# Optimization experiments

Measured on AMD Instinct MI355X. Metric: run time of the kernel, lower is better.

The kernel has to match this reference:

```python
import jax, jax.numpy as jnp
import numpy as np

DIM_IN = 1024
DIM_OUT = 1024
NUM_HEADS = 16
HEAD_DIM = DIM_OUT // NUM_HEADS


def setup_inputs() -> dict:
    key = jax.random.key(0)
    ks = jax.random.split(key, 7)
    s = 1.0 / np.sqrt(DIM_IN)
    x = jax.random.normal(ks[0], (4, 2048, DIM_IN), dtype=jnp.float32)
    Wq = jax.random.uniform(ks[1], (DIM_IN, DIM_OUT), jnp.float32, -s, s)
    bq = jax.random.uniform(ks[2], (DIM_OUT,), jnp.float32, -s, s)
    Wk = jax.random.uniform(ks[3], (DIM_IN, DIM_OUT), jnp.float32, -s, s)
    bk = jax.random.uniform(ks[4], (DIM_OUT,), jnp.float32, -s, s)
    Wv = jax.random.uniform(ks[5], (DIM_IN, DIM_OUT), jnp.float32, -s, s)
    bv = jax.random.uniform(ks[6], (DIM_OUT,), jnp.float32, -s, s)
    return {"x": x, "Wq": Wq, "bq": bq, "Wk": Wk, "bk": bk, "Wv": Wv, "bv": bv}


def reference(x, Wq, bq, Wk, bk, Wv, bv):
    B, S, _ = x.shape
    scale = HEAD_DIM ** 0.5
    # project and split heads: [B, H, S, Dh]
    def heads(W, b):
        return (x @ W + b).reshape(B, S, NUM_HEADS, HEAD_DIM).transpose(0, 2, 1, 3)
    q = heads(Wq, bq)
    k = heads(Wk, bk)
    v = heads(Wv, bv)
    scores = jnp.einsum("bhqd,bhkd->bhqk", q, k) / scale  # [B,H,S,S]
    attn = jax.nn.softmax(scores, axis=-1)
    out = jnp.einsum("bhqk,bhkd->bhqd", attn, v)
    return out.transpose(0, 2, 1, 3).reshape(B, S, DIM_OUT)
```

## Files before the change

### kernel.cpp

```cpp
#include <hip/hip_runtime.h>
#include <hip/hip_bf16.h>


#define DIM  1024
#define SEQ  2048
#define BATCH 4
#define NH   16
#define HD   64

typedef __bf16 bf16x8 __attribute__((ext_vector_type(8)));
typedef short  s16x4  __attribute__((ext_vector_type(4)));
typedef float  f32x4  __attribute__((ext_vector_type(4)));
typedef float  f32x16 __attribute__((ext_vector_type(16)));
typedef unsigned int uint4v __attribute__((ext_vector_type(4)));

static __device__ __forceinline__ f32x16 mfma32(bf16x8 a, bf16x8 b, f32x16 c) {
    return __builtin_amdgcn_mfma_f32_32x32x16_bf16(a, b, c, 0, 0, 0);
}

static __device__ __forceinline__ unsigned short f2b(float f) {
    __bf16 h = (__bf16)f;
    return __builtin_bit_cast(unsigned short, h);
}

static __device__ __forceinline__ void load_lds16(const unsigned short* g,
                                                  unsigned short* l) {
    __builtin_amdgcn_global_load_lds(
        (const __attribute__((address_space(1))) void*)g,
        (__attribute__((address_space(3))) void*)l, 16, 0, 0);
}

__global__ __launch_bounds__(256) void cvt_x_k(const float* __restrict__ x,
                                               unsigned short* __restrict__ xb) {
    size_t i = ((size_t)blockIdx.x * 256 + threadIdx.x) * 8;
    const f32x4* s = (const f32x4*)(x + i);
    f32x4 a0 = s[0], a1 = s[1];
    bf16x8 v;
    for (int j = 0; j < 4; j++) { v[j] = (__bf16)a0[j]; v[4 + j] = (__bf16)a1[j]; }
    *(bf16x8*)(xb + i) = v;
}

__global__ void transpose_w_k(const float* __restrict__ Wq,
                              const float* __restrict__ Wk,
                              const float* __restrict__ Wv,
                              unsigned short* __restrict__ Wt) {
    __shared__ unsigned short t[32][33];
    int z = blockIdx.z;
    const float* W = (z == 0) ? Wq : (z == 1) ? Wk : Wv;
    unsigned short* o = Wt + (size_t)z * DIM * DIM;
    int tx = threadIdx.x;
    int n0 = blockIdx.x * 32, k0 = blockIdx.y * 32;
    for (int j = threadIdx.y; j < 32; j += 8)
        t[j][tx] = f2b(W[(size_t)(k0 + j) * DIM + n0 + tx]);
    __syncthreads();
    for (int j = threadIdx.y; j < 32; j += 8)
        o[(size_t)(n0 + j) * DIM + k0 + tx] = t[tx][j];
}

__global__ __launch_bounds__(512) void qkv_gemm_k(
    const unsigned short* __restrict__ xb,
    const unsigned short* __restrict__ WtBase,
    const float* __restrict__ bq,
    const float* __restrict__ bk,
    const float* __restrict__ bv,
    unsigned short* __restrict__ Qo,
    unsigned short* __restrict__ Ko,
    unsigned short* __restrict__ Vto) {
    __shared__ __align__(16) unsigned short As[256 * 64];
    __shared__ __align__(16) unsigned short Bs[128 * 64];
    int tid = threadIdx.x, wave = tid >> 6, lane = tid & 63;
    int quad = lane >> 4, lc = lane & 15;
    int bid = blockIdx.x;
    int xcd = bid & 7, slot = bid >> 3;
    int pp = slot / 24, i = slot - pp * 24;
    int p = pp * 8 + xcd;
    int z = i >> 3, nx = i & 7;
    int m0 = p * 256, n0 = nx * 128;
    const unsigned short* Wt = WtBase + (size_t)z * DIM * DIM;
    int wm = (wave >> 1) * 64, wn = (wave & 1) * 64;
    int swzlo = lc & 7;

    f32x4 acc[4][4] = {};

    for (int k0 = 0; k0 < DIM; k0 += 64) {
        __syncthreads();
        #pragma unroll
        for (int pI = 0; pI < 4; pI++) {
            int c = tid + pI * 512, r = c >> 3, cc = (c & 7) ^ (r & 7);
            load_lds16(xb + (size_t)(m0 + r) * DIM + k0 + cc * 8, &As[c * 8]);
        }
        #pragma unroll
        for (int pI = 0; pI < 2; pI++) {
            int c = tid + pI * 512, r = c >> 3, cc = (c & 7) ^ (r & 7);
            load_lds16(Wt + (size_t)(n0 + r) * DIM + k0 + cc * 8, &Bs[c * 8]);
        }
        __syncthreads();
        #pragma unroll
        for (int kk = 0; kk < 2; kk++) {
            int off = ((kk * 4 + quad) ^ swzlo) * 8;
            bf16x8 af[4], bfr[4];
            for (int mt = 0; mt < 4; mt++)
                af[mt] = *(const bf16x8*)&As[(wm + mt * 16 + lc) * 64 + off];
            for (int nt = 0; nt < 4; nt++)
                bfr[nt] = *(const bf16x8*)&Bs[(wn + nt * 16 + lc) * 64 + off];
            for (int mt = 0; mt < 4; mt++)
                for (int nt = 0; nt < 4; nt++)
                    acc[mt][nt] = __builtin_amdgcn_mfma_f32_16x16x32_bf16(
                        af[mt], bfr[nt], acc[mt][nt], 0, 0, 0);
        }
    }

    const float* bias = (z == 0) ? bq : (z == 1) ? bk : bv;
    float scale = (z == 0) ? 0.18033688011112042f : 1.0f;

    if (z != 2) {
        for (int nt = 0; nt < 4; nt++) {
            int n = n0 + wn + nt * 16 + lc;
            float bvl = bias[n];
            int h = n >> 6, d = n & 63;
            for (int mt = 0; mt < 4; mt++) {
                for (int r = 0; r < 4; r++) {
                    int m = m0 + wm + mt * 16 + quad * 4 + r;
                    int b = m >> 11, s = m & 2047;
                    unsigned short ub = f2b((acc[mt][nt][r] + bvl) * scale);
                    if (z == 0)
                        Qo[((size_t)(b * NH + h) * SEQ + s) * HD + d] = ub;
                    else
                        Ko[((size_t)(b * NH + h) * SEQ + s) * HD + d] = ub;
                }
            }
        }
    } else {
        __syncthreads();
        unsigned short* T = As + wave * 1024;
        int h = (n0 + wn) >> 6;
        int d = lane;
        for (int mt = 0; mt < 4; mt++) {
            for (int nt = 0; nt < 4; nt++) {
                int n = n0 + wn + nt * 16 + lc;
                float bvl = bias[n];
                s16x4 v4;
                for (int r = 0; r < 4; r++)
                    v4[r] = (short)f2b(acc[mt][nt][r] + bvl);
                *(s16x4*)&T[(nt * 16 + lc) * 16 + quad * 4] = v4;
            }
            int s_base = m0 + wm + mt * 16;
            int b = s_base >> 11, sl = s_base & 2047;
            unsigned short* dst =
                Vto + ((size_t)(b * NH + h) * HD + d) * SEQ + sl;
            uint4v t0 = *(const uint4v*)&T[d * 16];
            uint4v t1 = *(const uint4v*)&T[d * 16 + 8];
            *(uint4v*)&dst[0] = t0;
            *(uint4v*)&dst[8] = t1;
        }
    }
}

__global__ __launch_bounds__(512) void attn_k(
    const unsigned short* __restrict__ Q,
    const unsigned short* __restrict__ K,
    const unsigned short* __restrict__ Vt,
    float* __restrict__ out) {
    __shared__ __align__(16) unsigned short KV[2 * 8192];

    int tid = threadIdx.x, wave = tid >> 6, lane = tid & 63;
    int l31 = lane & 31, hi = lane >> 5;
    int bid = blockIdx.x;
    int j = bid >> 3;
    int bh = (bid & 7) * 8 + (j >> 3);
    int qt = j & 7;
    int b = bh >> 4, h = bh & 15;
    const unsigned short* Qg = Q + ((size_t)bh * SEQ + qt * 256) * HD;
    const unsigned short* Kg = K + (size_t)bh * SEQ * HD;
    const unsigned short* Vg = Vt + (size_t)bh * HD * SEQ;

    int sr = tid >> 3, scc = tid & 7;
    int kcc = scc ^ ((sr ^ (sr >> 3)) & 7);

    bf16x8 qf[4];
    {
        const unsigned short* q0 = Qg + (size_t)(wave * 32 + l31) * HD + hi * 8;
        #pragma unroll
        for (int ds_ = 0; ds_ < 4; ds_++)
            qf[ds_] = *(const bf16x8*)(q0 + ds_ * 16);
    }

    f32x16 o[2] = {};
    f32x16 racc = {};
    bf16x8 ones8;
    #pragma unroll
    for (int t = 0; t < 8; t++) ones8[t] = (__bf16)1.0f;

    int swzK0 = ((l31 ^ (l31 >> 3)) & 7);
    int r32 = 32 + l31;
    int swzK1 = ((r32 ^ (r32 >> 3)) & 7);

    {
        unsigned short* Ks = KV;
        unsigned short* Vs = KV + 4096;
        load_lds16(Kg + (size_t)sr * HD + kcc * 8, &Ks[tid * 8]);
        load_lds16(Vg + (size_t)sr * SEQ + kcc * 8, &Vs[tid * 8]);
    }

    for (int t0 = 0; t0 < SEQ; t0 += 64) {
        int cur = (t0 >> 6) & 1;
        unsigned short* Ks = KV + cur * 8192;
        unsigned short* Vs = Ks + 4096;
        __syncthreads();

        if (t0 + 64 < SEQ) {
            unsigned short* Kn = KV + (cur ^ 1) * 8192;
            unsigned short* Vn = Kn + 4096;
            load_lds16(Kg + (size_t)(t0 + 64 + sr) * HD + kcc * 8, &Kn[tid * 8]);
            load_lds16(Vg + (size_t)sr * SEQ + (t0 + 64) + kcc * 8, &Vn[tid * 8]);
        }

        __builtin_amdgcn_s_setprio(1);
        #pragma unroll
        for (int kb = 0; kb < 2; kb++) {
            int krow = kb * 32 + l31;
            int ksw = (kb == 0) ? swzK0 : swzK1;
            f32x16 sc = {};
            #pragma unroll
            for (int ds_ = 0; ds_ < 4; ds_++) {
                bf16x8 kfrag = *(const bf16x8*)
                    &Ks[krow * 64 + ((ds_ * 2 + hi) ^ ksw) * 8];
                sc = mfma32(kfrag, qf[ds_], sc);
            }
            unsigned int W[8];
            #pragma unroll
            for (int rr = 0; rr < 8; rr++) {
                float p0 = __builtin_amdgcn_exp2f(sc[2 * rr]);
                float p1 = __builtin_amdgcn_exp2f(sc[2 * rr + 1]);
                W[rr] = ((unsigned)f2b(p1) << 16) | (unsigned)f2b(p0);
            }
            asm volatile("v_permlane32_swap_b32 %0, %1"
                         : "+v"(W[0]), "+v"(W[2]));
            asm volatile("v_permlane32_swap_b32 %0, %1"
                         : "+v"(W[1]), "+v"(W[3]));
            asm volatile("v_permlane32_swap_b32 %0, %1"
                         : "+v"(W[4]), "+v"(W[6]));
            asm volatile("v_permlane32_swap_b32 %0, %1"
                         : "+v"(W[5]), "+v"(W[7]));
            bf16x8 fA = __builtin_bit_cast(bf16x8,
                            (uint4v){W[0], W[1], W[2], W[3]});
            bf16x8 fB = __builtin_bit_cast(bf16x8,
                            (uint4v){W[4], W[5], W[6], W[7]});
            racc = mfma32(ones8, fA, racc);
            racc = mfma32(ones8, fB, racc);
            #pragma unroll
            for (int db = 0; db < 2; db++) {
                int vrow = db * 32 + l31;
                int vsw = (db == 0) ? swzK0 : swzK1;
                bf16x8 v0 = *(const bf16x8*)
                    &Vs[vrow * 64 + ((kb * 4 + hi) ^ vsw) * 8];
                bf16x8 v1 = *(const bf16x8*)
                    &Vs[vrow * 64 + ((kb * 4 + 2 + hi) ^ vsw) * 8];
                o[db] = mfma32(v0, fA, o[db]);
                o[db] = mfma32(v1, fB, o[db]);
            }
        }
        __builtin_amdgcn_s_setprio(0);
    }

    float inv = 1.0f / racc[0];

    float* orow = out + ((size_t)b * SEQ + qt * 256 + wave * 32 + l31) * DIM
                  + h * HD + hi * 4;
    #pragma unroll
    for (int db = 0; db < 2; db++) {
        #pragma unroll
        for (int rr = 0; rr < 4; rr++) {
            f32x4 s = { o[db][4 * rr], o[db][4 * rr + 1],
                        o[db][4 * rr + 2], o[db][4 * rr + 3] };
            s *= inv;
            *(f32x4*)&orow[db * 32 + rr * 8] = s;
        }
    }
}

extern "C" void kernel_launch(void* const* d_in, const int* in_sizes, int n_in,
                              void* d_out, int out_size, void* d_ws, size_t ws_size,
                              hipStream_t stream) {
    (void)in_sizes; (void)n_in; (void)out_size; (void)ws_size;
    const float* x  = (const float*)d_in[0];
    const float* Wq = (const float*)d_in[1];
    const float* bq = (const float*)d_in[2];
    const float* Wk = (const float*)d_in[3];
    const float* bk = (const float*)d_in[4];
    const float* Wv = (const float*)d_in[5];
    const float* bv = (const float*)d_in[6];

    char* ws = (char*)d_ws;
    unsigned short* Wt = (unsigned short*)ws;
    unsigned short* Qb = (unsigned short*)(ws + (size_t)6 * 1024 * 1024);
    unsigned short* Kb = Qb + (size_t)BATCH * NH * SEQ * HD;
    unsigned short* Vb = Kb + (size_t)BATCH * NH * SEQ * HD;
    unsigned short* xb = (unsigned short*)d_out;

    cvt_x_k<<<dim3(4096), dim3(256), 0, stream>>>(x, xb);
    transpose_w_k<<<dim3(32, 32, 3), dim3(32, 8), 0, stream>>>(Wq, Wk, Wv, Wt);
    qkv_gemm_k<<<dim3(768), dim3(512), 0, stream>>>(xb, Wt, bq, bk, bv, Qb, Kb, Vb);
    attn_k<<<dim3(512), dim3(512), 0, stream>>>(Qb, Kb, Vb, (float*)d_out);
}
```

Baseline: 239.8 us.

## Double attention KV tile to 128 keys and merge prep kernels into one launch

The attention kernel now stages 128 keys per iteration instead of 64, with 64KB of LDS for the double buffer, a new V swizzle over 16 chunks per row, and half as many barriers per sequence. The x conversion and weight transpose kernels are fused into a single launch, removing one kernel-launch gap. The bf16 packing of P now uses a vector cast, which may let the compiler emit a packed convert. The larger LDS footprint may lower occupancy of the attention kernel.

After: 237.1 us. About the same (-1.1%).

```diff
diff --git a/kernel.cpp b/kernel.cpp
--- a/kernel.cpp
+++ b/kernel.cpp
@@ -9,6 +9,7 @@
 #define HD   64
 
 typedef __bf16 bf16x8 __attribute__((ext_vector_type(8)));
+typedef __bf16 bf16x2 __attribute__((ext_vector_type(2)));
 typedef short  s16x4  __attribute__((ext_vector_type(4)));
 typedef float  f32x4  __attribute__((ext_vector_type(4)));
 typedef float  f32x16 __attribute__((ext_vector_type(16)));
@@ -30,31 +31,33 @@
         (__attribute__((address_space(3))) void*)l, 16, 0, 0);
 }
 
-__global__ __launch_bounds__(256) void cvt_x_k(const float* __restrict__ x,
-                                               unsigned short* __restrict__ xb) {
-    size_t i = ((size_t)blockIdx.x * 256 + threadIdx.x) * 8;
-    const f32x4* s = (const f32x4*)(x + i);
-    f32x4 a0 = s[0], a1 = s[1];
-    bf16x8 v;
-    for (int j = 0; j < 4; j++) { v[j] = (__bf16)a0[j]; v[4 + j] = (__bf16)a1[j]; }
-    *(bf16x8*)(xb + i) = v;
-}
-
-__global__ void transpose_w_k(const float* __restrict__ Wq,
-                              const float* __restrict__ Wk,
-                              const float* __restrict__ Wv,
-                              unsigned short* __restrict__ Wt) {
+__global__ __launch_bounds__(256) void prep_k(
+    const float* __restrict__ x, unsigned short* __restrict__ xb,
+    const float* __restrict__ Wq, const float* __restrict__ Wk,
+    const float* __restrict__ Wv, unsigned short* __restrict__ Wt) {
     __shared__ unsigned short t[32][33];
-    int z = blockIdx.z;
-    const float* W = (z == 0) ? Wq : (z == 1) ? Wk : Wv;
-    unsigned short* o = Wt + (size_t)z * DIM * DIM;
-    int tx = threadIdx.x;
-    int n0 = blockIdx.x * 32, k0 = blockIdx.y * 32;
-    for (int j = threadIdx.y; j < 32; j += 8)
-        t[j][tx] = f2b(W[(size_t)(k0 + j) * DIM + n0 + tx]);
-    __syncthreads();
-    for (int j = threadIdx.y; j < 32; j += 8)
-        o[(size_t)(n0 + j) * DIM + k0 + tx] = t[tx][j];
+    int bid = blockIdx.x, tid = threadIdx.x;
+    if (bid < 4096) {
+        size_t i = ((size_t)bid * 256 + tid) * 8;
+        const f32x4* s = (const f32x4*)(x + i);
+        f32x4 a0 = s[0], a1 = s[1];
+        bf16x8 v;
+        for (int j = 0; j < 4; j++) { v[j] = (__bf16)a0[j]; v[4 + j] = (__bf16)a1[j]; }
+        *(bf16x8*)(xb + i) = v;
+    } else {
+        int r = bid - 4096;
+        int z = r >> 10;
+        int by = (r >> 5) & 31, bx = r & 31;
+        const float* W = (z == 0) ? Wq : (z == 1) ? Wk : Wv;
+        unsigned short* o = Wt + (size_t)z * DIM * DIM;
+        int tx = tid & 31, ty = tid >> 5;
+        int n0 = bx * 32, k0 = by * 32;
+        for (int j = ty; j < 32; j += 8)
+            t[j][tx] = f2b(W[(size_t)(k0 + j) * DIM + n0 + tx]);
+        __syncthreads();
+        for (int j = ty; j < 32; j += 8)
+            o[(size_t)(n0 + j) * DIM + k0 + tx] = t[tx][j];
+    }
 }
 
 __global__ __launch_bounds__(512) void qkv_gemm_k(
@@ -161,7 +164,7 @@
     const unsigned short* __restrict__ K,
     const unsigned short* __restrict__ Vt,
     float* __restrict__ out) {
-    __shared__ __align__(16) unsigned short KV[2 * 8192];
+    __shared__ __align__(16) unsigned short KV[2 * 16384];
 
     int tid = threadIdx.x, wave = tid >> 6, lane = tid & 63;
     int l31 = lane & 31, hi = lane >> 5;
@@ -174,8 +177,14 @@
     const unsigned short* Kg = K + (size_t)bh * SEQ * HD;
     const unsigned short* Vg = Vt + (size_t)bh * HD * SEQ;
 
-    int sr = tid >> 3, scc = tid & 7;
-    int kcc = scc ^ ((sr ^ (sr >> 3)) & 7);
+    int kr0 = tid >> 3, kc0 = tid & 7;
+    int ks0 = kc0 ^ ((kr0 ^ (kr0 >> 3)) & 7);
+    int kr1 = (tid + 512) >> 3, kc1 = tid & 7;
+    int ks1 = kc1 ^ ((kr1 ^ (kr1 >> 3)) & 7);
+    int vr0 = tid >> 4, vc0 = tid & 15;
+    int vs0 = (vc0 & 8) | ((vc0 & 7) ^ ((vr0 ^ (vr0 >> 3)) & 7));
+    int vr1 = (tid + 512) >> 4, vc1 = tid & 15;
+    int vs1 = (vc1 & 8) | ((vc1 & 7) ^ ((vr1 ^ (vr1 >> 3)) & 7));
 
     bf16x8 qf[4];
     {
@@ -197,29 +206,37 @@
 
     {
         unsigned short* Ks = KV;
-        unsigned short* Vs = KV + 4096;
-        load_lds16(Kg + (size_t)sr * HD + kcc * 8, &Ks[tid * 8]);
-        load_lds16(Vg + (size_t)sr * SEQ + kcc * 8, &Vs[tid * 8]);
-    }
-
-    for (int t0 = 0; t0 < SEQ; t0 += 64) {
-        int cur = (t0 >> 6) & 1;
-        unsigned short* Ks = KV + cur * 8192;
-        unsigned short* Vs = Ks + 4096;
-        __syncthreads();
-
-        if (t0 + 64 < SEQ) {
-            unsigned short* Kn = KV + (cur ^ 1) * 8192;
-            unsigned short* Vn = Kn + 4096;
-            load_lds16(Kg + (size_t)(t0 + 64 + sr) * HD + kcc * 8, &Kn[tid * 8]);
-            load_lds16(Vg + (size_t)sr * SEQ + (t0 + 64) + kcc * 8, &Vn[tid * 8]);
+        unsigned short* Vs = KV + 8192;
+        load_lds16(Kg + (size_t)kr0 * HD + ks0 * 8, &Ks[tid * 8]);
+        load_lds16(Kg + (size_t)kr1 * HD + ks1 * 8, &Ks[(tid + 512) * 8]);
+        load_lds16(Vg + (size_t)vr0 * SEQ + vs0 * 8, &Vs[tid * 8]);
+        load_lds16(Vg + (size_t)vr1 * SEQ + vs1 * 8, &Vs[(tid + 512) * 8]);
+    }
+
+    for (int t0 = 0; t0 < SEQ; t0 += 128) {
+        int cur = (t0 >> 7) & 1;
+        unsigned short* Ks = KV + cur * 16384;
+        unsigned short* Vs = Ks + 8192;
+        __syncthreads();
+
+        if (t0 + 128 < SEQ) {
+            unsigned short* Kn = KV + (cur ^ 1) * 16384;
+            unsigned short* Vn = Kn + 8192;
+            load_lds16(Kg + (size_t)(t0 + 128 + kr0) * HD + ks0 * 8,
+                       &Kn[tid * 8]);
+            load_lds16(Kg + (size_t)(t0 + 128 + kr1) * HD + ks1 * 8,
+                       &Kn[(tid + 512) * 8]);
+            load_lds16(Vg + (size_t)vr0 * SEQ + (t0 + 128) + vs0 * 8,
+                       &Vn[tid * 8]);
+            load_lds16(Vg + (size_t)vr1 * SEQ + (t0 + 128) + vs1 * 8,
+                       &Vn[(tid + 512) * 8]);
         }
 
         __builtin_amdgcn_s_setprio(1);
         #pragma unroll
-        for (int kb = 0; kb < 2; kb++) {
+        for (int kb = 0; kb < 4; kb++) {
             int krow = kb * 32 + l31;
-            int ksw = (kb == 0) ? swzK0 : swzK1;
+            int ksw = (kb & 1) ? swzK1 : swzK0;
             f32x16 sc = {};
             #pragma unroll
             for (int ds_ = 0; ds_ < 4; ds_++) {
@@ -232,7 +249,8 @@
             for (int rr = 0; rr < 8; rr++) {
                 float p0 = __builtin_amdgcn_exp2f(sc[2 * rr]);
                 float p1 = __builtin_amdgcn_exp2f(sc[2 * rr + 1]);
-                W[rr] = ((unsigned)f2b(p1) << 16) | (unsigned)f2b(p0);
+                bf16x2 pk; pk[0] = (__bf16)p0; pk[1] = (__bf16)p1;
+                W[rr] = __builtin_bit_cast(unsigned int, pk);
             }
             asm volatile("v_permlane32_swap_b32 %0, %1"
                          : "+v"(W[0]), "+v"(W[2]));
@@ -252,10 +270,11 @@
             for (int db = 0; db < 2; db++) {
                 int vrow = db * 32 + l31;
                 int vsw = (db == 0) ? swzK0 : swzK1;
-                bf16x8 v0 = *(const bf16x8*)
-                    &Vs[vrow * 64 + ((kb * 4 + hi) ^ vsw) * 8];
-                bf16x8 v1 = *(const bf16x8*)
-                    &Vs[vrow * 64 + ((kb * 4 + 2 + hi) ^ vsw) * 8];
+                int rawA = kb * 4 + hi, rawB = kb * 4 + 2 + hi;
+                int cA = (rawA & 8) | ((rawA & 7) ^ vsw);
+                int cB = (rawB & 8) | ((rawB & 7) ^ vsw);
+                bf16x8 v0 = *(const bf16x8*)&Vs[vrow * 128 + cA * 8];
+                bf16x8 v1 = *(const bf16x8*)&Vs[vrow * 128 + cB * 8];
                 o[db] = mfma32(v0, fA, o[db]);
                 o[db] = mfma32(v1, fB, o[db]);
             }
@@ -298,8 +317,7 @@
     unsigned short* Vb = Kb + (size_t)BATCH * NH * SEQ * HD;
     unsigned short* xb = (unsigned short*)d_out;
 
-    cvt_x_k<<<dim3(4096), dim3(256), 0, stream>>>(x, xb);
-    transpose_w_k<<<dim3(32, 32, 3), dim3(32, 8), 0, stream>>>(Wq, Wk, Wv, Wt);
+    prep_k<<<dim3(7168), dim3(256), 0, stream>>>(x, xb, Wq, Wk, Wv, Wt);
     qkv_gemm_k<<<dim3(768), dim3(512), 0, stream>>>(xb, Wt, bq, bk, bv, Qb, Kb, Vb);
     attn_k<<<dim3(512), dim3(512), 0, stream>>>(Qb, Kb, Vb, (float*)d_out);
 }
```

## Double-buffer QKV GEMM LDS with K-step 32, merge prep kernels, pack bf16

Applied to the files above, without the earlier changes.

The QKV projection GEMM now uses two LDS buffers with a K-step of 32 and a matching swizzle. The next tile is prefetched while MFMAs run on the current one, which drops one barrier per iteration. The x conversion and weight transpose kernels are merged into one launch to save launch overhead. The attention kernel now packs exp results with a native bf16x2 conversion. Risks: a smaller K-step doubles the loop iterations, and the single-barrier scheme depends on asynchronous LDS loads completing before the barrier.

New measurement: 239.3 us. Within noise of the previous version (-0.2%).

```diff
diff --git a/kernel.cpp b/kernel.cpp
--- a/kernel.cpp
+++ b/kernel.cpp
@@ -9,6 +9,7 @@
 #define HD   64
 
 typedef __bf16 bf16x8 __attribute__((ext_vector_type(8)));
+typedef __bf16 bf16x2 __attribute__((ext_vector_type(2)));
 typedef short  s16x4  __attribute__((ext_vector_type(4)));
 typedef float  f32x4  __attribute__((ext_vector_type(4)));
 typedef float  f32x16 __attribute__((ext_vector_type(16)));
@@ -30,31 +31,33 @@
         (__attribute__((address_space(3))) void*)l, 16, 0, 0);
 }
 
-__global__ __launch_bounds__(256) void cvt_x_k(const float* __restrict__ x,
-                                               unsigned short* __restrict__ xb) {
-    size_t i = ((size_t)blockIdx.x * 256 + threadIdx.x) * 8;
-    const f32x4* s = (const f32x4*)(x + i);
-    f32x4 a0 = s[0], a1 = s[1];
-    bf16x8 v;
-    for (int j = 0; j < 4; j++) { v[j] = (__bf16)a0[j]; v[4 + j] = (__bf16)a1[j]; }
-    *(bf16x8*)(xb + i) = v;
-}
-
-__global__ void transpose_w_k(const float* __restrict__ Wq,
-                              const float* __restrict__ Wk,
-                              const float* __restrict__ Wv,
-                              unsigned short* __restrict__ Wt) {
+__global__ __launch_bounds__(256) void prep_k(
+    const float* __restrict__ x, unsigned short* __restrict__ xb,
+    const float* __restrict__ Wq, const float* __restrict__ Wk,
+    const float* __restrict__ Wv, unsigned short* __restrict__ Wt) {
     __shared__ unsigned short t[32][33];
-    int z = blockIdx.z;
-    const float* W = (z == 0) ? Wq : (z == 1) ? Wk : Wv;
-    unsigned short* o = Wt + (size_t)z * DIM * DIM;
-    int tx = threadIdx.x;
-    int n0 = blockIdx.x * 32, k0 = blockIdx.y * 32;
-    for (int j = threadIdx.y; j < 32; j += 8)
-        t[j][tx] = f2b(W[(size_t)(k0 + j) * DIM + n0 + tx]);
-    __syncthreads();
-    for (int j = threadIdx.y; j < 32; j += 8)
-        o[(size_t)(n0 + j) * DIM + k0 + tx] = t[tx][j];
+    int bid = blockIdx.x, tid = threadIdx.x;
+    if (bid < 4096) {
+        size_t i = ((size_t)bid * 256 + tid) * 8;
+        const f32x4* s = (const f32x4*)(x + i);
+        f32x4 a0 = s[0], a1 = s[1];
+        bf16x8 v;
+        for (int j = 0; j < 4; j++) { v[j] = (__bf16)a0[j]; v[4 + j] = (__bf16)a1[j]; }
+        *(bf16x8*)(xb + i) = v;
+    } else {
+        int r = bid - 4096;
+        int z = r >> 10;
+        int by = (r >> 5) & 31, bx = r & 31;
+        const float* W = (z == 0) ? Wq : (z == 1) ? Wk : Wv;
+        unsigned short* o = Wt + (size_t)z * DIM * DIM;
+        int tx = tid & 31, ty = tid >> 5;
+        int n0 = bx * 32, k0 = by * 32;
+        for (int j = ty; j < 32; j += 8)
+            t[j][tx] = f2b(W[(size_t)(k0 + j) * DIM + n0 + tx]);
+        __syncthreads();
+        for (int j = ty; j < 32; j += 8)
+            o[(size_t)(n0 + j) * DIM + k0 + tx] = t[tx][j];
+    }
 }
 
 __global__ __launch_bounds__(512) void qkv_gemm_k(
@@ -66,8 +69,7 @@
     unsigned short* __restrict__ Qo,
     unsigned short* __restrict__ Ko,
     unsigned short* __restrict__ Vto) {
-    __shared__ __align__(16) unsigned short As[256 * 64];
-    __shared__ __align__(16) unsigned short Bs[128 * 64];
+    __shared__ __align__(16) unsigned short AB[2 * 12288];
     int tid = threadIdx.x, wave = tid >> 6, lane = tid & 63;
     int quad = lane >> 4, lc = lane & 15;
     int bid = blockIdx.x;
@@ -78,36 +80,52 @@
     int m0 = p * 256, n0 = nx * 128;
     const unsigned short* Wt = WtBase + (size_t)z * DIM * DIM;
     int wm = (wave >> 1) * 64, wn = (wave & 1) * 64;
-    int swzlo = lc & 7;
+    int off = ((quad ^ ((lc >> 1) & 3))) * 8;
+
+    int ar0 = tid >> 2, ac0 = (tid & 3) ^ ((ar0 >> 1) & 3);
+    int ar1 = (tid + 512) >> 2, ac1 = (tid & 3) ^ ((ar1 >> 1) & 3);
+    int br0 = tid >> 2, bc0 = (tid & 3) ^ ((br0 >> 1) & 3);
 
     f32x4 acc[4][4] = {};
 
-    for (int k0 = 0; k0 < DIM; k0 += 64) {
+    {
+        unsigned short* As = AB;
+        unsigned short* Bs = AB + 8192;
+        load_lds16(xb + (size_t)(m0 + ar0) * DIM + ac0 * 8, &As[tid * 8]);
+        load_lds16(xb + (size_t)(m0 + ar1) * DIM + ac1 * 8, &As[(tid + 512) * 8]);
+        load_lds16(Wt + (size_t)(n0 + br0) * DIM + bc0 * 8, &Bs[tid * 8]);
+    }
+
+    for (int k0 = 0; k0 < DIM; k0 += 32) {
+        int cur = (k0 >> 5) & 1;
+        unsigned short* As = AB + cur * 12288;
+        unsigned short* Bs = As + 8192;
         __syncthreads();
-        #pragma unroll
-        for (int pI = 0; pI < 4; pI++) {
-            int c = tid + pI * 512, r = c >> 3, cc = (c & 7) ^ (r & 7);
-            load_lds16(xb + (size_t)(m0 + r) * DIM + k0 + cc * 8, &As[c * 8]);
-        }
-        #pragma unroll
-        for (int pI = 0; pI < 2; pI++) {
-            int c = tid + pI * 512, r = c >> 3, cc = (c & 7) ^ (r & 7);
-            load_lds16(Wt + (size_t)(n0 + r) * DIM + k0 + cc * 8, &Bs[c * 8]);
-        }
-        __syncthreads();
-        #pragma unroll
-        for (int kk = 0; kk < 2; kk++) {
-            int off = ((kk * 4 + quad) ^ swzlo) * 8;
-            bf16x8 af[4], bfr[4];
-            for (int mt = 0; mt < 4; mt++)
-                af[mt] = *(const bf16x8*)&As[(wm + mt * 16 + lc) * 64 + off];
+
+        if (k0 + 32 < DIM) {
+            unsigned short* An = AB + (cur ^ 1) * 12288;
+            unsigned short* Bn = An + 8192;
+            load_lds16(xb + (size_t)(m0 + ar0) * DIM + k0 + 32 + ac0 * 8,
+                       &An[tid * 8]);
+            load_lds16(xb + (size_t)(m0 + ar1) * DIM + k0 + 32 + ac1 * 8,
+                       &An[(tid + 512) * 8]);
+            load_lds16(Wt + (size_t)(n0 + br0) * DIM + k0 + 32 + bc0 * 8,
+                       &Bn[tid * 8]);
+        }
+
+        bf16x8 af[4], bfr[4];
+        #pragma unroll
+        for (int mt = 0; mt < 4; mt++)
+            af[mt] = *(const bf16x8*)&As[(wm + mt * 16 + lc) * 32 + off];
+        #pragma unroll
+        for (int nt = 0; nt < 4; nt++)
+            bfr[nt] = *(const bf16x8*)&Bs[(wn + nt * 16 + lc) * 32 + off];
+        #pragma unroll
+        for (int mt = 0; mt < 4; mt++)
+            #pragma unroll
             for (int nt = 0; nt < 4; nt++)
-                bfr[nt] = *(const bf16x8*)&Bs[(wn + nt * 16 + lc) * 64 + off];
-            for (int mt = 0; mt < 4; mt++)
-                for (int nt = 0; nt < 4; nt++)
-                    acc[mt][nt] = __builtin_amdgcn_mfma_f32_16x16x32_bf16(
-                        af[mt], bfr[nt], acc[mt][nt], 0, 0, 0);
-        }
+                acc[mt][nt] = __builtin_amdgcn_mfma_f32_16x16x32_bf16(
+                    af[mt], bfr[nt], acc[mt][nt], 0, 0, 0);
     }
 
     const float* bias = (z == 0) ? bq : (z == 1) ? bk : bv;
@@ -132,7 +150,7 @@
         }
     } else {
         __syncthreads();
-        unsigned short* T = As + wave * 1024;
+        unsigned short* T = AB + wave * 1024;
         int h = (n0 + wn) >> 6;
         int d = lane;
         for (int mt = 0; mt < 4; mt++) {
@@ -232,7 +250,8 @@
             for (int rr = 0; rr < 8; rr++) {
                 float p0 = __builtin_amdgcn_exp2f(sc[2 * rr]);
                 float p1 = __builtin_amdgcn_exp2f(sc[2 * rr + 1]);
-                W[rr] = ((unsigned)f2b(p1) << 16) | (unsigned)f2b(p0);
+                bf16x2 pk; pk[0] = (__bf16)p0; pk[1] = (__bf16)p1;
+                W[rr] = __builtin_bit_cast(unsigned int, pk);
             }
             asm volatile("v_permlane32_swap_b32 %0, %1"
                          : "+v"(W[0]), "+v"(W[2]));
@@ -298,8 +317,7 @@
     unsigned short* Vb = Kb + (size_t)BATCH * NH * SEQ * HD;
     unsigned short* xb = (unsigned short*)d_out;
 
-    cvt_x_k<<<dim3(4096), dim3(256), 0, stream>>>(x, xb);
-    transpose_w_k<<<dim3(32, 32, 3), dim3(32, 8), 0, stream>>>(Wq, Wk, Wv, Wt);
+    prep_k<<<dim3(7168), dim3(256), 0, stream>>>(x, xb, Wq, Wk, Wv, Wt);
     qkv_gemm_k<<<dim3(768), dim3(512), 0, stream>>>(xb, Wt, bq, bk, bv, Qb, Kb, Vb);
     attn_k<<<dim3(512), dim3(512), 0, stream>>>(Qb, Kb, Vb, (float*)d_out);
 }
```
